# Kernel tuning notes

Hardware: AMD Instinct MI355X
Metric: run time of the kernel (lower is better)

## Reference

```python
import jax, jax.numpy as jnp
import numpy as np

PAIRS = np.array([[0, 4], [1, 5], [2, 6], [3, 7], [0, 5], [1, 4], [2, 7], [3, 6]])


def setup_inputs() -> dict:
    key = jax.random.key(0)
    ks = jax.random.split(key, 40)
    rn = lambda k, shape: (jax.random.normal(k, shape, jnp.float32) * 0.05)
    inp = {
        "waiting": jax.random.uniform(ks[0], (1, 8), jnp.float32),
        "phase": jax.random.uniform(ks[1], (1, 8), jnp.float32),
        "wtime_mu": jax.random.uniform(ks[2], (1, 8), jnp.float32),
        "wtime_sigma": jax.random.uniform(ks[3], (1, 8), jnp.float32),
        "wtime_max": jax.random.uniform(ks[4], (1, 8), jnp.float32),
        "i_position": jax.random.uniform(ks[5], (1, 1), jnp.float32),
        "j_position": jax.random.uniform(ks[6], (1, 1), jnp.float32),
        # NN_demand: 14 -> 256 -> 32 -> 4
        "d_w1": rn(ks[7], (256, 14)), "d_b1": rn(ks[8], (256,)),
        "d_w2": rn(ks[9], (32, 256)), "d_b2": rn(ks[10], (32,)),
        "d_w3": rn(ks[11], (4, 32)), "d_b3": rn(ks[12], (4,)),
        # NN_coupled_demand: 8 -> 128 -> 32 -> 4
        "c_w1": rn(ks[13], (128, 8)), "c_b1": rn(ks[14], (128,)),
        "c_w2": rn(ks[15], (32, 128)), "c_b2": rn(ks[16], (32,)),
        "c_w3": rn(ks[17], (4, 32)), "c_b3": rn(ks[18], (4,)),
        # Conv_D: 1x1 convs 8 -> 256 -> 32 -> 2
        "dD_w1": rn(ks[19], (256, 8)), "dD_b1": rn(ks[20], (256,)),
        "dD_w2": rn(ks[21], (32, 256)), "dD_b2": rn(ks[22], (32,)),
        "dD_w3": rn(ks[23], (2, 32)), "dD_b3": rn(ks[24], (2,)),
        # Conv_C: 1x1 convs 3 -> 256 -> 32 -> 8, then (1,7) conv 8 -> 1
        "cC_w1": rn(ks[25], (256, 3)), "cC_b1": rn(ks[26], (256,)),
        "cC_w2": rn(ks[27], (32, 256)), "cC_b2": rn(ks[28], (32,)),
        "cC_w3": rn(ks[29], (8, 32)), "cC_b3": rn(ks[30], (8,)),
        "cC_w4": rn(ks[31], (8, 7)), "cC_b4": rn(ks[32], (1,)),
    }
    return inp


def _mlp3(x, w1, b1, w2, b2, w3, b3):
    h = jax.nn.relu(x @ w1.T + b1)
    h = jax.nn.relu(h @ w2.T + b2)
    return h @ w3.T + b3


def _frap_forward(waiting, phase, wtime_mu, wtime_sigma, wtime_max, i_position, j_position,
                  d_w1, d_b1, d_w2, d_b2, d_w3, d_b3,
                  c_w1, c_b1, c_w2, c_b2, c_w3, c_b3,
                  dD_w1, dD_b1, dD_w2, dD_b2, dD_w3, dD_b3,
                  cC_w1, cC_b1, cC_w2, cC_b2, cC_w3, cC_b3, cC_w4, cC_b4):
    pairs = jnp.asarray(PAIRS)
    # per-lane demand features: (8, 14) = [i, j, mu_l, sigma_l, max_l, wait_l, phase(8)]
    feat = jnp.concatenate([
        jnp.broadcast_to(i_position[0], (8, 1)),
        jnp.broadcast_to(j_position[0], (8, 1)),
        wtime_mu[0, :, None], wtime_sigma[0, :, None],
        wtime_max[0, :, None], waiting[0, :, None],
        jnp.broadcast_to(phase[0][None, :], (8, 8)),
    ], axis=1)
    demand = _mlp3(feat, d_w1, d_b1, d_w2, d_b2, d_w3, d_b3)  # (8, 4)
    # coupled demand per phase pair: (8, 8) -> (8, 4)
    vec = jnp.concatenate([demand[pairs[:, 0]], demand[pairs[:, 1]]], axis=1)
    dp = _mlp3(vec, c_w1, c_b1, c_w2, c_b2, c_w3, c_b3)  # (8, 4)
    # D tensor (8, 8, 7): D[0:4, i, k] = dp[i]; D[4:8, i, k] = dp[j(k)], j(k)=k + (k>=i)
    k = jnp.arange(7)
    i = jnp.arange(8)
    j_idx = k[None, :] + (k[None, :] >= i[:, None]).astype(jnp.int32)  # (8, 7)
    top = jnp.broadcast_to(dp.T[:, :, None], (4, 8, 7))
    bot = jnp.transpose(dp[j_idx], (2, 0, 1))  # (4, 8, 7)
    D = jnp.concatenate([top, bot], axis=0)  # (8, 8, 7)
    # Conv_D: 1x1 convs are channel matmuls on (C, H, W)
    h = jax.nn.relu(jnp.einsum('oc,chw->ohw', dD_w1, D) + dD_b1[:, None, None])
    h = jax.nn.relu(jnp.einsum('oc,chw->ohw', dD_w2, h) + dD_b2[:, None, None])
    H_d = jnp.einsum('oc,chw->ohw', dD_w3, h) + dD_b3[:, None, None]  # (2, 8, 7)
    comp = jnp.zeros((1, 8, 7), H_d.dtype)
    H_c = jnp.concatenate([H_d, comp], axis=0)  # (3, 8, 7)
    # Conv_C
    h = jax.nn.relu(jnp.einsum('oc,chw->ohw', cC_w1, H_c) + cC_b1[:, None, None])
    h = jax.nn.relu(jnp.einsum('oc,chw->ohw', cC_w2, h) + cC_b2[:, None, None])
    h = jax.nn.relu(jnp.einsum('oc,chw->ohw', cC_w3, h) + cC_b3[:, None, None])  # (8, 8, 7)
    # conv4: kernel (1,7), out (1, 8, 1); return C[0, :, 0] -> (8,)
    out = jnp.einsum('cw,chw->h', cC_w4, h) + cC_b4[0]
    return out


def reference(waiting, phase, wtime_mu, wtime_sigma, wtime_max, i_position, j_position,
              d_w1, d_b1, d_w2, d_b2, d_w3, d_b3,
              c_w1, c_b1, c_w2, c_b2, c_w3, c_b3,
              dD_w1, dD_b1, dD_w2, dD_b2, dD_w3, dD_b3,
              cC_w1, cC_b1, cC_w2, cC_b2, cC_w3, cC_b3, cC_w4, cC_b4):
    return _frap_forward(waiting, phase, wtime_mu, wtime_sigma, wtime_max, i_position, j_position,
                         d_w1, d_b1, d_w2, d_b2, d_w3, d_b3,
                         c_w1, c_b1, c_w2, c_b2, c_w3, c_b3,
                         dD_w1, dD_b1, dD_w2, dD_b2, dD_w3, dD_b3,
                         cC_w1, cC_b1, cC_w2, cC_b2, cC_w3, cC_b3, cC_w4, cC_b4)
```

## Files before the change

kernel.cpp:

```cpp
#include <hip/hip_runtime.h>


#define DEV __device__ __forceinline__

#define WAVE_SYNC() do { \
    asm volatile("s_waitcnt lgkmcnt(0)" ::: "memory"); \
    __builtin_amdgcn_sched_barrier(0); \
} while (0)

DEV float dot4a(float acc, float4 a, float4 b) {
    acc = fmaf(a.x, b.x, acc);
    acc = fmaf(a.y, b.y, acc);
    acc = fmaf(a.z, b.z, acc);
    acc = fmaf(a.w, b.w, acc);
    return acc;
}

DEV float warm_arr(const float* __restrict__ p, int n4, int id, float sink) {
    const float4* p4 = (const float4*)p;
    for (int i = id; i < n4; i += 384) {
        float4 v = p4[i];
        sink += v.x + v.y + v.z + v.w;
    }
    return sink;
}

DEV void conv_h2_vec(const float* __restrict__ big, const float* __restrict__ w2g,
                     const float* __restrict__ b2g, float* __restrict__ mid, int t)
{
    int kq = t & 1;
    int u  = t >> 1;
    int ch = u >> 3, sl = u & 7;
    float a0 = 0.0f, a1 = 0.0f, a2 = 0.0f, a3 = 0.0f;
    if (sl < 7) {
        const float4* wp = (const float4*)(w2g + ch * 256) + kq * 32;
        const float* hrow = big + (sl << 8);
#pragma unroll 2
        for (int g = 0; g < 32; g += 4) {
            int gg = kq * 32 + g;
            float4 w0 = wp[g + 0], w1 = wp[g + 1], w2 = wp[g + 2], w3 = wp[g + 3];
            float4 h0 = *(const float4*)(hrow + (((gg + 0) ^ sl) << 2));
            float4 h1 = *(const float4*)(hrow + (((gg + 1) ^ sl) << 2));
            float4 h2 = *(const float4*)(hrow + (((gg + 2) ^ sl) << 2));
            float4 h3v = *(const float4*)(hrow + (((gg + 3) ^ sl) << 2));
            a0 = dot4a(a0, h0, w0);
            a1 = dot4a(a1, h1, w1);
            a2 = dot4a(a2, h2, w2);
            a3 = dot4a(a3, h3v, w3);
        }
    }
    float r = (a0 + a1) + (a2 + a3);
    r += __shfl_xor(r, 1);
    if (sl < 7 && kq == 0)
        mid[ch * 7 + sl] = fmaxf(r + b2g[ch], 0.0f);
}

__global__ __launch_bounds__(512, 1) void frap_kernel(
    const float* __restrict__ waiting, const float* __restrict__ phase,
    const float* __restrict__ wtime_mu, const float* __restrict__ wtime_sigma,
    const float* __restrict__ wtime_max,
    const float* __restrict__ i_pos, const float* __restrict__ j_pos,
    const float* __restrict__ d_w1, const float* __restrict__ d_b1,
    const float* __restrict__ d_w2, const float* __restrict__ d_b2,
    const float* __restrict__ d_w3, const float* __restrict__ d_b3,
    const float* __restrict__ c_w1, const float* __restrict__ c_b1,
    const float* __restrict__ c_w2, const float* __restrict__ c_b2,
    const float* __restrict__ c_w3, const float* __restrict__ c_b3,
    const float* __restrict__ dD_w1, const float* __restrict__ dD_b1,
    const float* __restrict__ dD_w2, const float* __restrict__ dD_b2,
    const float* __restrict__ dD_w3, const float* __restrict__ dD_b3,
    const float* __restrict__ cC_w1, const float* __restrict__ cC_b1,
    const float* __restrict__ cC_w2, const float* __restrict__ cC_b2,
    const float* __restrict__ cC_w3, const float* __restrict__ cC_b3,
    const float* __restrict__ cC_w4, const float* __restrict__ cC_b4,
    float* __restrict__ out)
{
    __shared__ __align__(16) float sm[4096];
    const int t  = threadIdx.x;
    const int wg = blockIdx.x;
    const int wv = t >> 6;
    const int ln = t & 63;

    float* feat16 = sm;
    float* dh1  = sm + 128;
    float* dh2  = sm + 2176;
    float* dem  = sm + 2432;
    float* ch1  = sm + 2464;
    float* ch2  = sm + 3488;
    float* dp   = sm + 3968;
    float* convh   = sm;
    float* mid     = sm + 1792;
    float* partial = sm + 2016;

    if (wv < 2) {
        const int wbase = wv * 4;
        {
            int idx = wv * 64 + ln;
            int l = idx >> 4, c = idx & 15;
            float v = 0.0f;
            if      (c == 0) v = i_pos[0];
            else if (c == 1) v = j_pos[0];
            else if (c == 2) v = wtime_mu[l];
            else if (c == 3) v = wtime_sigma[l];
            else if (c == 4) v = wtime_max[l];
            else if (c == 5) v = waiting[l];
            else if (c < 14) v = phase[c - 6];
            feat16[idx] = v;
        }
        WAVE_SYNC();

        for (int q = 0; q < 4; ++q) {
            int o = q * 64 + ln;
            const float* w = d_w1 + o * 14;
            float w0 = w[0], w1 = w[1], w2 = w[2], w3 = w[3], w4 = w[4];
            float w5 = w[5], w6 = w[6], w7 = w[7], w8 = w[8], w9 = w[9];
            float wa = w[10], wb = w[11], wc = w[12], wd = w[13];
            float bias = d_b1[o];
#pragma unroll
            for (int r = 0; r < 4; ++r) {
                int l = wbase + r;
                const float4* f4 = (const float4*)(feat16 + l * 16);
                float4 f0 = f4[0], f1 = f4[1], f2 = f4[2], f3 = f4[3];
                float acc = bias;
                acc = fmaf(f0.x, w0, acc); acc = fmaf(f0.y, w1, acc);
                acc = fmaf(f0.z, w2, acc); acc = fmaf(f0.w, w3, acc);
                acc = fmaf(f1.x, w4, acc); acc = fmaf(f1.y, w5, acc);
                acc = fmaf(f1.z, w6, acc); acc = fmaf(f1.w, w7, acc);
                acc = fmaf(f2.x, w8, acc); acc = fmaf(f2.y, w9, acc);
                acc = fmaf(f2.z, wa, acc); acc = fmaf(f2.w, wb, acc);
                acc = fmaf(f3.x, wc, acc); acc = fmaf(f3.y, wd, acc);
                dh1[l * 256 + o] = fmaxf(acc, 0.0f);
            }
        }
        WAVE_SYNC();

        {
            int o = ln & 31, lh = ln >> 5;
            int r0 = wbase + lh * 2, r1 = r0 + 1;
            float acc0 = 0.0f, acc1 = 0.0f;
            const float4* w4p = (const float4*)(d_w2 + o * 256);
#pragma unroll 4
            for (int cb = 0; cb < 64; ++cb) {
                float4 w = w4p[cb];
                float4 h0 = *(const float4*)(dh1 + r0 * 256 + cb * 4);
                float4 h1 = *(const float4*)(dh1 + r1 * 256 + cb * 4);
                acc0 = dot4a(acc0, h0, w);
                acc1 = dot4a(acc1, h1, w);
            }
            float b = d_b2[o];
            dh2[r0 * 32 + o] = fmaxf(acc0 + b, 0.0f);
            dh2[r1 * 32 + o] = fmaxf(acc1 + b, 0.0f);
        }
        WAVE_SYNC();

        if (ln < 16) {
            int l = wbase + (ln >> 2), o = ln & 3;
            const float4* w = (const float4*)(d_w3 + o * 32);
            const float4* h = (const float4*)(dh2 + l * 32);
            float acc = d_b3[o];
#pragma unroll
            for (int g = 0; g < 8; ++g) acc = dot4a(acc, h[g], w[g]);
            dem[l * 4 + o] = acc;
        }
    } else {
        int id = t - 128;
        float snk = 0.0f;
        snk = warm_arr(d_w1,  896, id, snk);
        snk = warm_arr(d_b1,   64, id, snk);
        snk = warm_arr(d_w2, 2048, id, snk);
        snk = warm_arr(d_b2,    8, id, snk);
        snk = warm_arr(d_w3,   32, id, snk);
        snk = warm_arr(d_b3,    1, id, snk);
        snk = warm_arr(c_w1,  256, id, snk);
        snk = warm_arr(c_b1,   32, id, snk);
        snk = warm_arr(c_w2, 1024, id, snk);
        snk = warm_arr(c_b2,    8, id, snk);
        snk = warm_arr(c_w3,   32, id, snk);
        snk = warm_arr(c_b3,    1, id, snk);
        asm volatile("" :: "v"(snk));
    }
    __syncthreads();

    if (wv < 2) {
        const int pbase = wv * 4;
        for (int rep = 0; rep < 2; ++rep) {
            int o = rep * 64 + ln;
            const float4* w = (const float4*)(c_w1 + o * 8);
            float4 w0 = w[0], w1 = w[1];
            float bias = c_b1[o];
#pragma unroll
            for (int pp = 0; pp < 4; ++pp) {
                int p = pbase + pp;
                int a0 = p & 3;
                int a1 = (p < 4) ? (4 + (p & 3)) : (4 + ((p & 3) ^ 1));
                float4 va = *(const float4*)(dem + a0 * 4);
                float4 vb = *(const float4*)(dem + a1 * 4);
                float acc = dot4a(dot4a(bias, va, w0), vb, w1);
                ch1[p * 128 + o] = fmaxf(acc, 0.0f);
            }
        }
        WAVE_SYNC();

        {
            int o = ln & 31, lh = ln >> 5;
            int r0 = pbase + lh * 2, r1 = r0 + 1;
            float acc0 = 0.0f, acc1 = 0.0f;
            const float4* w4p = (const float4*)(c_w2 + o * 128);
#pragma unroll 4
            for (int cb = 0; cb < 32; ++cb) {
                float4 w = w4p[cb];
                float4 h0 = *(const float4*)(ch1 + r0 * 128 + cb * 4);
                float4 h1 = *(const float4*)(ch1 + r1 * 128 + cb * 4);
                acc0 = dot4a(acc0, h0, w);
                acc1 = dot4a(acc1, h1, w);
            }
            float b = c_b2[o];
            ch2[r0 * 32 + o] = fmaxf(acc0 + b, 0.0f);
            ch2[r1 * 32 + o] = fmaxf(acc1 + b, 0.0f);
        }
        WAVE_SYNC();

        if (ln < 16) {
            int p = pbase + (ln >> 2), o = ln & 3;
            const float4* w = (const float4*)(c_w3 + o * 32);
            const float4* h = (const float4*)(ch2 + p * 32);
            float acc = c_b3[o];
#pragma unroll
            for (int g = 0; g < 8; ++g) acc = dot4a(acc, h[g], w[g]);
            dp[p * 4 + o] = acc;
        }
    } else {
        int id = t - 128;
        float snk = 0.0f;
        snk = warm_arr(dD_w1,  512, id, snk);
        snk = warm_arr(dD_b1,   64, id, snk);
        snk = warm_arr(dD_w2, 2048, id, snk);
        snk = warm_arr(dD_b2,    8, id, snk);
        snk = warm_arr(dD_w3,   16, id, snk);
        snk = warm_arr(cC_w1,  192, id, snk);
        snk = warm_arr(cC_b1,   64, id, snk);
        snk = warm_arr(cC_w2, 2048, id, snk);
        snk = warm_arr(cC_b2,    8, id, snk);
        snk = warm_arr(cC_w3,   64, id, snk);
        snk = warm_arr(cC_b3,    2, id, snk);
        snk = warm_arr(cC_w4,   14, id, snk);
        asm volatile("" :: "v"(snk));
    }
    __syncthreads();

    {
        const float4* dp4 = (const float4*)dp;
        int o = t & 255;
        const float4* wrow = (const float4*)(dD_w1 + o * 8);
        float4 w0 = wrow[0], w1 = wrow[1];
        float bias = dD_b1[o];
        float4 di = dp4[wg];
#pragma unroll
        for (int it = 0; it < 4; ++it) {
            int sl = (t >> 8) + it * 2;
            if (sl < 7) {
                int j = sl + (sl >= wg ? 1 : 0);
                float acc = dot4a(dot4a(bias, di, w0), dp4[j], w1);
                convh[(sl << 8) + (((o >> 2) ^ sl) << 2) + (o & 3)] = fmaxf(acc, 0.0f);
            }
        }
    }
    __syncthreads();

    conv_h2_vec(convh, dD_w2, dD_b2, mid, t);
    __syncthreads();

    if (wv < 7) {
        const int w = wv;
        float s00 = 0.0f, s01 = 0.0f, s02 = 0.0f, s03 = 0.0f;
        float s10 = 0.0f, s11 = 0.0f, s12 = 0.0f, s13 = 0.0f;
#pragma unroll
        for (int cc = 0; cc < 8; ++cc) {
            float m0 = mid[(0 * 8 + cc) * 7 + w];
            float m1 = mid[(1 * 8 + cc) * 7 + w];
            float m2 = mid[(2 * 8 + cc) * 7 + w];
            float m3 = mid[(3 * 8 + cc) * 7 + w];
            s00 = fmaf(m0, dD_w3[0 * 32 + 0 * 8 + cc], s00);
            s01 = fmaf(m1, dD_w3[0 * 32 + 1 * 8 + cc], s01);
            s02 = fmaf(m2, dD_w3[0 * 32 + 2 * 8 + cc], s02);
            s03 = fmaf(m3, dD_w3[0 * 32 + 3 * 8 + cc], s03);
            s10 = fmaf(m0, dD_w3[1 * 32 + 0 * 8 + cc], s10);
            s11 = fmaf(m1, dD_w3[1 * 32 + 1 * 8 + cc], s11);
            s12 = fmaf(m2, dD_w3[1 * 32 + 2 * 8 + cc], s12);
            s13 = fmaf(m3, dD_w3[1 * 32 + 3 * 8 + cc], s13);
        }
        float hd0 = ((s00 + s01) + (s02 + s03)) + dD_b3[0];
        float hd1 = ((s10 + s11) + (s12 + s13)) + dD_b3[1];
#pragma unroll
        for (int q = 0; q < 4; ++q) {
            int o = q * 64 + ln;
            float acc = fmaf(hd1, cC_w1[o * 3 + 1],
                             fmaf(hd0, cC_w1[o * 3], cC_b1[o]));
            convh[(w << 8) + (((o >> 2) ^ w) << 2) + (o & 3)] = fmaxf(acc, 0.0f);
        }
    }
    __syncthreads();

    conv_h2_vec(convh, cC_w2, cC_b2, mid, t);
    __syncthreads();

    if (wv < 7 && ln < 8) {
        const int w = wv;
        const int o = ln;
        float s0 = 0.0f, s1 = 0.0f, s2 = 0.0f, s3 = 0.0f;
#pragma unroll
        for (int cc = 0; cc < 8; ++cc) {
            s0 = fmaf(mid[(0 * 8 + cc) * 7 + w], cC_w3[o * 32 + 0 * 8 + cc], s0);
            s1 = fmaf(mid[(1 * 8 + cc) * 7 + w], cC_w3[o * 32 + 1 * 8 + cc], s1);
            s2 = fmaf(mid[(2 * 8 + cc) * 7 + w], cC_w3[o * 32 + 2 * 8 + cc], s2);
            s3 = fmaf(mid[(3 * 8 + cc) * 7 + w], cC_w3[o * 32 + 3 * 8 + cc], s3);
        }
        float h3v = fmaxf(((s0 + s1) + (s2 + s3)) + cC_b3[o], 0.0f);
        float p = cC_w4[o * 7 + w] * h3v;
        p += __shfl_xor(p, 1);
        p += __shfl_xor(p, 2);
        p += __shfl_xor(p, 4);
        if (o == 0) partial[w] = p;
    }
    __syncthreads();

    if (t == 0) {
        float s = cC_b4[0];
#pragma unroll
        for (int w = 0; w < 7; ++w) s += partial[w];
        out[wg] = s;
    }
}

extern "C" void kernel_launch(void* const* d_in, const int* in_sizes, int n_in,
                              void* d_out, int out_size, void* d_ws, size_t ws_size,
                              hipStream_t stream) {
    (void)in_sizes; (void)n_in; (void)d_ws; (void)ws_size; (void)out_size;
    const float* a[33];
    for (int i = 0; i < 33; ++i) a[i] = (const float*)d_in[i];
    frap_kernel<<<dim3(8), dim3(512), 0, stream>>>(
        a[0], a[1], a[2], a[3], a[4], a[5], a[6],
        a[7], a[8], a[9], a[10], a[11], a[12],
        a[13], a[14], a[15], a[16], a[17], a[18],
        a[19], a[20], a[21], a[22], a[23], a[24],
        a[25], a[26], a[27], a[28], a[29], a[30], a[31], a[32],
        (float*)d_out);
}
```

Baseline: 25.88 us.

## Add helper blocks to prefetch weights with rotated start offsets

Launches eight extra workgroups that return early after touching every weight array, so the data is pulled into L2/MALL before the compute blocks need it. Every prefetch loop, in both the helper blocks and the compute blocks' idle waves, now starts at a different rotated offset per block. This spreads the concurrent misses across different cache lines instead of having all blocks request the same addresses together. The cost is extra global load traffic and more workgroups to launch.

After: 26.72 us. 3.3% more time.

```diff
diff --git a/kernel.cpp b/kernel.cpp
--- a/kernel.cpp
+++ b/kernel.cpp
@@ -16,10 +16,14 @@
     return acc;
 }
 
-DEV float warm_arr(const float* __restrict__ p, int n4, int id, float sink) {
+DEV float warm_rot(const float* __restrict__ p, int n4, int id, int stride,
+                   int r16, float sink) {
     const float4* p4 = (const float4*)p;
-    for (int i = id; i < n4; i += 384) {
-        float4 v = p4[i];
+    int start = (n4 * r16) >> 4;
+    for (int i = id; i < n4; i += stride) {
+        int k = i + start;
+        if (k >= n4) k -= n4;
+        float4 v = p4[k];
         sink += v.x + v.y + v.z + v.w;
     }
     return sink;
@@ -75,9 +79,43 @@
     const float* __restrict__ cC_w4, const float* __restrict__ cC_b4,
     float* __restrict__ out)
 {
+    const int wgid = blockIdx.x;
+    const int t  = threadIdx.x;
+
+    if (wgid >= 8) {
+        const int r16 = ((wgid - 8) << 1) + 1;
+        float snk = 0.0f;
+        snk = warm_rot(d_w1,  896, t, 512, r16, snk);
+        snk = warm_rot(d_b1,   64, t, 512, r16, snk);
+        snk = warm_rot(d_w2, 2048, t, 512, r16, snk);
+        snk = warm_rot(d_b2,    8, t, 512, r16, snk);
+        snk = warm_rot(d_w3,   32, t, 512, r16, snk);
+        snk = warm_rot(d_b3,    1, t, 512, r16, snk);
+        snk = warm_rot(c_w1,  256, t, 512, r16, snk);
+        snk = warm_rot(c_b1,   32, t, 512, r16, snk);
+        snk = warm_rot(c_w2, 1024, t, 512, r16, snk);
+        snk = warm_rot(c_b2,    8, t, 512, r16, snk);
+        snk = warm_rot(c_w3,   32, t, 512, r16, snk);
+        snk = warm_rot(c_b3,    1, t, 512, r16, snk);
+        snk = warm_rot(dD_w1,  512, t, 512, r16, snk);
+        snk = warm_rot(dD_b1,   64, t, 512, r16, snk);
+        snk = warm_rot(dD_w2, 2048, t, 512, r16, snk);
+        snk = warm_rot(dD_b2,    8, t, 512, r16, snk);
+        snk = warm_rot(dD_w3,   16, t, 512, r16, snk);
+        snk = warm_rot(cC_w1,  192, t, 512, r16, snk);
+        snk = warm_rot(cC_b1,   64, t, 512, r16, snk);
+        snk = warm_rot(cC_w2, 2048, t, 512, r16, snk);
+        snk = warm_rot(cC_b2,    8, t, 512, r16, snk);
+        snk = warm_rot(cC_w3,   64, t, 512, r16, snk);
+        snk = warm_rot(cC_b3,    2, t, 512, r16, snk);
+        snk = warm_rot(cC_w4,   14, t, 512, r16, snk);
+        asm volatile("" :: "v"(snk));
+        return;
+    }
+
     __shared__ __align__(16) float sm[4096];
-    const int t  = threadIdx.x;
-    const int wg = blockIdx.x;
+    const int wg = wgid;
+    const int r16 = wg << 1;
     const int wv = t >> 6;
     const int ln = t & 63;
 
@@ -165,18 +203,18 @@
     } else {
         int id = t - 128;
         float snk = 0.0f;
-        snk = warm_arr(d_w1,  896, id, snk);
-        snk = warm_arr(d_b1,   64, id, snk);
-        snk = warm_arr(d_w2, 2048, id, snk);
-        snk = warm_arr(d_b2,    8, id, snk);
-        snk = warm_arr(d_w3,   32, id, snk);
-        snk = warm_arr(d_b3,    1, id, snk);
-        snk = warm_arr(c_w1,  256, id, snk);
-        snk = warm_arr(c_b1,   32, id, snk);
-        snk = warm_arr(c_w2, 1024, id, snk);
-        snk = warm_arr(c_b2,    8, id, snk);
-        snk = warm_arr(c_w3,   32, id, snk);
-        snk = warm_arr(c_b3,    1, id, snk);
+        snk = warm_rot(d_w1,  896, id, 384, r16, snk);
+        snk = warm_rot(d_b1,   64, id, 384, r16, snk);
+        snk = warm_rot(d_w2, 2048, id, 384, r16, snk);
+        snk = warm_rot(d_b2,    8, id, 384, r16, snk);
+        snk = warm_rot(d_w3,   32, id, 384, r16, snk);
+        snk = warm_rot(d_b3,    1, id, 384, r16, snk);
+        snk = warm_rot(c_w1,  256, id, 384, r16, snk);
+        snk = warm_rot(c_b1,   32, id, 384, r16, snk);
+        snk = warm_rot(c_w2, 1024, id, 384, r16, snk);
+        snk = warm_rot(c_b2,    8, id, 384, r16, snk);
+        snk = warm_rot(c_w3,   32, id, 384, r16, snk);
+        snk = warm_rot(c_b3,    1, id, 384, r16, snk);
         asm volatile("" :: "v"(snk));
     }
     __syncthreads();
@@ -232,18 +270,18 @@
     } else {
         int id = t - 128;
         float snk = 0.0f;
-        snk = warm_arr(dD_w1,  512, id, snk);
-        snk = warm_arr(dD_b1,   64, id, snk);
-        snk = warm_arr(dD_w2, 2048, id, snk);
-        snk = warm_arr(dD_b2,    8, id, snk);
-        snk = warm_arr(dD_w3,   16, id, snk);
-        snk = warm_arr(cC_w1,  192, id, snk);
-        snk = warm_arr(cC_b1,   64, id, snk);
-        snk = warm_arr(cC_w2, 2048, id, snk);
-        snk = warm_arr(cC_b2,    8, id, snk);
-        snk = warm_arr(cC_w3,   64, id, snk);
-        snk = warm_arr(cC_b3,    2, id, snk);
-        snk = warm_arr(cC_w4,   14, id, snk);
+        snk = warm_rot(dD_w1,  512, id, 384, r16, snk);
+        snk = warm_rot(dD_b1,   64, id, 384, r16, snk);
+        snk = warm_rot(dD_w2, 2048, id, 384, r16, snk);
+        snk = warm_rot(dD_b2,    8, id, 384, r16, snk);
+        snk = warm_rot(dD_w3,   16, id, 384, r16, snk);
+        snk = warm_rot(cC_w1,  192, id, 384, r16, snk);
+        snk = warm_rot(cC_b1,   64, id, 384, r16, snk);
+        snk = warm_rot(cC_w2, 2048, id, 384, r16, snk);
+        snk = warm_rot(cC_b2,    8, id, 384, r16, snk);
+        snk = warm_rot(cC_w3,   64, id, 384, r16, snk);
+        snk = warm_rot(cC_b3,    2, id, 384, r16, snk);
+        snk = warm_rot(cC_w4,   14, id, 384, r16, snk);
         asm volatile("" :: "v"(snk));
     }
     __syncthreads();
@@ -338,7 +376,7 @@
     (void)in_sizes; (void)n_in; (void)d_ws; (void)ws_size; (void)out_size;
     const float* a[33];
     for (int i = 0; i < 33; ++i) a[i] = (const float*)d_in[i];
-    frap_kernel<<<dim3(8), dim3(512), 0, stream>>>(
+    frap_kernel<<<dim3(16), dim3(512), 0, stream>>>(
         a[0], a[1], a[2], a[3], a[4], a[5], a[6],
         a[7], a[8], a[9], a[10], a[11], a[12],
         a[13], a[14], a[15], a[16], a[17], a[18],
```
